# Kernel optimization log

Hardware: AMD Instinct MI355X
Metric: run time of the kernel (lower is better)

The kernel has to match this reference:

```python
import jax, jax.numpy as jnp
import numpy as np

B, S, D, H = 2, 2048, 1024, 16
HD = D // H

def setup_inputs() -> dict:
    key = jax.random.key(0)
    ks = jax.random.split(key, 6)
    s = 1.0 / np.sqrt(D)
    return {
        "inputs": jax.random.normal(ks[0], (B, S, D), dtype=jnp.float32),
        "Wq": jax.random.normal(ks[1], (D, D), dtype=jnp.float32) * s,
        "Wk": jax.random.normal(ks[2], (D, D), dtype=jnp.float32) * s,
        "Wv": jax.random.normal(ks[3], (D, D), dtype=jnp.float32) * s,
        "Wo": jax.random.normal(ks[4], (D, D), dtype=jnp.float32) * s,
        "bo": jax.random.normal(ks[5], (D,), dtype=jnp.float32) * 0.01,
    }

def reference(inputs, Wq, Wk, Wv, Wo, bo):
    b, n, _ = inputs.shape
    # Linear projections (torch Linear: x @ W.T), reshape to [b, H, n, hd]
    def proj(W):
        return (inputs @ W.T).reshape(b, n, H, HD).transpose(0, 2, 1, 3)
    q, k, v = proj(Wq), proj(Wk), proj(Wv)
    scores = jnp.einsum('bhqd,bhkd->bhqk', q, k)  # [b,H,n,n]
    causal = jnp.triu(jnp.ones((n, n), dtype=bool), k=1)
    scores = jnp.where(causal, -jnp.inf, scores)
    w = jax.nn.softmax(scores / np.sqrt(HD), axis=-1)
    ctx = jnp.einsum('bhqk,bhkd->bhqd', w, v)
    ctx = ctx.transpose(0, 2, 1, 3).reshape(b, n, D)
    return ctx @ Wo.T + bo
```

## Files before the change

### kernel.cpp

```cpp
#include <hip/hip_runtime.h>
#include <hip/hip_bf16.h>
#include <stdint.h>

#define B_   2
#define S_   2048
#define D_   1024
#define H_   16
#define LOG2E 1.4426950408889634f

using f32x4  = __attribute__((ext_vector_type(4))) float;
using short8 = __attribute__((ext_vector_type(8))) short;

__device__ __forceinline__ unsigned short f2bf(float x) {
    unsigned u = __builtin_bit_cast(unsigned, x);
    u += 0x7fffu + ((u >> 16) & 1u);
    return (unsigned short)(u >> 16);
}

__device__ __forceinline__ unsigned cvt_pk_bf16(float lo, float hi) {
    unsigned r;
    asm("v_cvt_pk_bf16_f32 %0, %1, %2" : "=v"(r) : "v"(lo), "v"(hi));
    return r;
}

__device__ __forceinline__ float fast_exp2(float x) {
    float r;
    asm("v_exp_f32 %0, %1" : "=v"(r) : "v"(x));
    return r;
}

__device__ __forceinline__ float fast_rcp(float x) {
    float r;
    asm("v_rcp_f32 %0, %1" : "=v"(r) : "v"(x));
    return r;
}

__device__ __forceinline__ void gll16(const void* g, void* l) {
    __builtin_amdgcn_global_load_lds(
        (const __attribute__((address_space(1))) void*)(uintptr_t)g,
        (__attribute__((address_space(3))) void*)(uint32_t)(uintptr_t)l,
        16, 0, 0);
}

#define MFMA_BF16(a, b, c) __builtin_amdgcn_mfma_f32_16x16x32_bf16((a), (b), (c), 0, 0, 0)

__global__ __launch_bounds__(256)
void conv_all_kernel(const float* __restrict__ X,
                     const float* __restrict__ Wq, const float* __restrict__ Wk,
                     const float* __restrict__ Wv, const float* __restrict__ Wo,
                     short* __restrict__ Xb, short* __restrict__ Wqkv,
                     short* __restrict__ Wob) {
    const int bid = blockIdx.x;
    const float* src;
    short* dst;
    float sc = 1.0f;
    int i;
    if (bid < 2048) {
        src = X; dst = Xb; i = bid * 256 + threadIdx.x;
    } else {
        int wv = bid - 2048;
        int which = wv >> 9;
        src = (which == 0) ? Wq : (which == 1) ? Wk : (which == 2) ? Wv : Wo;
        dst = (which == 3) ? Wob : (Wqkv + (size_t)which * D_ * D_);
        if (which == 0) sc = 0.125f * LOG2E;
        i = (wv & 511) * 256 + threadIdx.x;
    }
    const float4* s4 = (const float4*)src;
    float4 a = s4[i * 2];
    float4 b = s4[i * 2 + 1];
    union { unsigned short u[8]; short8 v; } o;
    o.u[0] = f2bf(a.x * sc); o.u[1] = f2bf(a.y * sc); o.u[2] = f2bf(a.z * sc); o.u[3] = f2bf(a.w * sc);
    o.u[4] = f2bf(b.x * sc); o.u[5] = f2bf(b.y * sc); o.u[6] = f2bf(b.z * sc); o.u[7] = f2bf(b.w * sc);
    ((short8*)dst)[i] = o.v;
}

__global__ __launch_bounds__(256, 3)
void gemm_qkv_m97_kernel(const short* __restrict__ X, const short* __restrict__ Wqkv,
                         short* __restrict__ Qo, short* __restrict__ Ko,
                         short* __restrict__ VTo)
{
    __shared__ short sA[128 * 64];
    __shared__ short sB[128 * 64];
    const int cid = blockIdx.x;
    const int swz = (cid & 7) * 96 + (cid >> 3);
    const int n0 = (swz % 24) * 128;
    const int m0 = (swz / 24) * 128;
    const int tid = threadIdx.x, lane = tid & 63, w = tid >> 6;
    const int wm = w & 1, wn = w >> 1;
    const int l15 = lane & 15, lg = lane >> 4;

    const f32x4 z4 = {0.f, 0.f, 0.f, 0.f};
    f32x4 acc[4][4];
    #pragma unroll
    for (int i = 0; i < 4; ++i)
        #pragma unroll
        for (int j = 0; j < 4; ++j) acc[i][j] = z4;

    for (int kt = 0; kt < 16; ++kt) {
        const int k0 = kt << 6;
        #pragma unroll
        for (int it = 0; it < 4; ++it) {
            int g = it * 256 + tid;
            int r = g >> 3, s = g & 7;
            int sb = s ^ (r & 7);
            int dst = (it * 256 + w * 64) * 16;
            gll16(X    + (size_t)(m0 + r) * D_ + k0 + sb * 8, (char*)sA + dst);
            gll16(Wqkv + (size_t)(n0 + r) * D_ + k0 + sb * 8, (char*)sB + dst);
        }
        __syncthreads();
        #pragma unroll
        for (int ks = 0; ks < 2; ++ks) {
            short8 af[4], bf[4];
            #pragma unroll
            for (int i = 0; i < 4; ++i) {
                int r = wm * 64 + i * 16 + l15;
                af[i] = *(const short8*)(sA + r * 64 + ((((ks << 2) + lg) ^ (r & 7)) << 3));
            }
            #pragma unroll
            for (int j = 0; j < 4; ++j) {
                int r = wn * 64 + j * 16 + l15;
                bf[j] = *(const short8*)(sB + r * 64 + ((((ks << 2) + lg) ^ (r & 7)) << 3));
            }
            __builtin_amdgcn_s_setprio(1);
            #pragma unroll
            for (int i = 0; i < 4; ++i)
                #pragma unroll
                for (int j = 0; j < 4; ++j)
                    acc[i][j] = MFMA_BF16(af[i], bf[j], acc[i][j]);
            __builtin_amdgcn_s_setprio(0);
        }
        __syncthreads();
    }

    const int z = n0 >> 10;
    if (z < 2) {
        short* Out = (z == 0) ? Qo : Ko;
        #pragma unroll
        for (int j = 0; j < 4; ++j) {
            int n = n0 + wn * 64 + j * 16 + l15;
            int h = (n >> 6) & 15, hd = n & 63;
            #pragma unroll
            for (int i = 0; i < 4; ++i)
                #pragma unroll
                for (int r = 0; r < 4; ++r) {
                    int m = m0 + wm * 64 + i * 16 + lg * 4 + r;
                    int b = m >> 11, s = m & (S_ - 1);
                    Out[(((size_t)b * H_ + h) * S_ + s) * 64 + hd] = (short)f2bf(acc[i][j][r]);
                }
        }
    } else {
        #pragma unroll
        for (int j = 0; j < 4; ++j) {
            int n = n0 + wn * 64 + j * 16 + l15;
            int h = (n >> 6) & 15, hd = n & 63;
            #pragma unroll
            for (int i = 0; i < 4; ++i) {
                int m = m0 + wm * 64 + i * 16 + lg * 4;
                int b = m >> 11, s0 = m & (S_ - 1);
                union { unsigned u32[2]; unsigned long long q64; } pk;
                pk.u32[0] = cvt_pk_bf16(acc[i][j][0], acc[i][j][1]);
                pk.u32[1] = cvt_pk_bf16(acc[i][j][2], acc[i][j][3]);
                *(unsigned long long*)(VTo + (((size_t)b * H_ + h) * 64 + hd) * S_ + s0) = pk.q64;
            }
        }
    }
}

__global__ __launch_bounds__(512, 4)
void gemm_out_kernel(const short* __restrict__ CTX, const short* __restrict__ Wob,
                     const float* __restrict__ bias, float* __restrict__ out)
{
    __shared__ short sA[2][128 * 64];
    __shared__ short sB[2][128 * 64];
    const int cid = blockIdx.y * 8 + blockIdx.x;
    const int swz = (cid & 7) * 32 + (cid >> 3);
    const int n0 = (swz & 7) * 128;
    const int m0 = (swz >> 3) * 128;
    const int tid = threadIdx.x, lane = tid & 63, w = tid >> 6;
    const int wm = w >> 2, wn = w & 3;
    const int l15 = lane & 15, lg = lane >> 4;

#define STAGE_O(buf, kt) do {                                                  \
        int k0_ = (kt) << 6;                                                   \
        _Pragma("unroll")                                                      \
        for (int it_ = 0; it_ < 2; ++it_) {                                    \
            int g_ = it_ * 512 + tid;                                          \
            int r_ = g_ >> 3, s_ = g_ & 7;                                     \
            int sb_ = s_ ^ (r_ & 7);                                           \
            int dst_ = (it_ * 512 + w * 64) * 16;                              \
            gll16(CTX + (size_t)(m0 + r_) * D_ + k0_ + sb_ * 8,                \
                  (char*)sA[buf] + dst_);                                      \
            gll16(Wob + (size_t)(n0 + r_) * D_ + k0_ + sb_ * 8,                \
                  (char*)sB[buf] + dst_);                                      \
        }                                                                      \
    } while (0)

    const f32x4 z4 = {0.f, 0.f, 0.f, 0.f};
    f32x4 acc[4][2];
    #pragma unroll
    for (int i = 0; i < 4; ++i)
        #pragma unroll
        for (int j = 0; j < 2; ++j) acc[i][j] = z4;

    STAGE_O(0, 0);
    STAGE_O(1, 1);

    for (int t = 0; t < 16; ++t) {
        if (t < 15) { asm volatile("s_waitcnt vmcnt(4)" ::: "memory"); }
        else        { asm volatile("s_waitcnt vmcnt(0)" ::: "memory"); }
        __builtin_amdgcn_sched_barrier(0);
        __builtin_amdgcn_s_barrier();
        __builtin_amdgcn_sched_barrier(0);
        const short* a  = sA[t & 1];
        const short* bm = sB[t & 1];
        #pragma unroll
        for (int ks = 0; ks < 2; ++ks) {
            short8 af[4], bf[2];
            #pragma unroll
            for (int i = 0; i < 4; ++i) {
                int r = wm * 64 + i * 16 + l15;
                af[i] = *(const short8*)(a + r * 64 + ((((ks << 2) + lg) ^ (r & 7)) << 3));
            }
            #pragma unroll
            for (int j = 0; j < 2; ++j) {
                int r = wn * 32 + j * 16 + l15;
                bf[j] = *(const short8*)(bm + r * 64 + ((((ks << 2) + lg) ^ (r & 7)) << 3));
            }
            __builtin_amdgcn_s_setprio(1);
            #pragma unroll
            for (int i = 0; i < 4; ++i)
                #pragma unroll
                for (int j = 0; j < 2; ++j)
                    acc[i][j] = MFMA_BF16(af[i], bf[j], acc[i][j]);
            __builtin_amdgcn_s_setprio(0);
        }
        asm volatile("s_waitcnt lgkmcnt(0)" ::: "memory");
        __builtin_amdgcn_sched_barrier(0);
        __builtin_amdgcn_s_barrier();
        __builtin_amdgcn_sched_barrier(0);
        if (t + 2 < 16) STAGE_O(t & 1, t + 2);
    }
#undef STAGE_O

    #pragma unroll
    for (int j = 0; j < 2; ++j) {
        int n = n0 + wn * 32 + j * 16 + l15;
        float bn = bias[n];
        #pragma unroll
        for (int i = 0; i < 4; ++i)
            #pragma unroll
            for (int r = 0; r < 4; ++r) {
                int m = m0 + wm * 64 + i * 16 + lg * 4 + r;
                out[(size_t)m * D_ + n] = acc[i][j][r] + bn;
            }
    }
}

__global__ __launch_bounds__(256, 4)
void attn_kernel(const short* __restrict__ Q, const short* __restrict__ K,
                 const short* __restrict__ VT, short* __restrict__ CTX)
{
    __shared__ short Kb[2][4096];
    __shared__ short Vb[2][4096];
    __shared__ char  Pl[4 * 2048];
    const int idx = blockIdx.x;
    const int k4  = idx >> 8;
    const int u   = idx & 255;
    const int v   = u >> 5;
    const int bh  = u & 31;
    const int ht  = (k4 == 0) ? v : (k4 == 1) ? (15 - v)
                  : (k4 == 2) ? (16 + v) : (31 - v);
    const int b  = bh >> 4, h = bh & 15;
    const int tid = threadIdx.x, lane = tid & 63, w = tid >> 6;
    const int l15 = lane & 15, lg = lane >> 4;
    const short* Qg = Q  + (size_t)bh * S_ * 64;
    const short* Kg = K  + (size_t)bh * S_ * 64;
    const short* Vg = VT + (size_t)bh * 64 * S_;
    char* Pw = Pl + w * 2048;

    const int qb = ht * 64 + w * 16;
    const int nt = ht + 1;

#define STAGE_KV(bufidx, ktile) do {                                         \
        int kt64_ = (ktile) << 6;                                            \
        _Pragma("unroll")                                                    \
        for (int it_ = 0; it_ < 2; ++it_) {                                  \
            int g_ = it_ * 256 + tid;                                        \
            int row_ = g_ >> 3, jb_ = g_ & 7;                                \
            int sj_ = jb_ ^ (row_ & 7);                                      \
            int base_ = (it_ * 256 + w * 64) * 16;                           \
            gll16(Kg + (size_t)(kt64_ + row_) * 64 + sj_ * 8,                \
                  (char*)Kb[bufidx] + base_);                                \
            gll16(Vg + (size_t)row_ * S_ + kt64_ + sj_ * 8,                  \
                  (char*)Vb[bufidx] + base_);                                \
        }                                                                    \
    } while (0)

    short8 qf[2];
    #pragma unroll
    for (int ks = 0; ks < 2; ++ks)
        qf[ks] = *(const short8*)(Qg + (size_t)(qb + l15) * 64 + ks * 32 + lg * 8);

    const short8 ones8 = { (short)0x3F80, (short)0x3F80, (short)0x3F80, (short)0x3F80,
                           (short)0x3F80, (short)0x3F80, (short)0x3F80, (short)0x3F80 };
    const f32x4 z4 = {0.f, 0.f, 0.f, 0.f};
    f32x4 o[4];
    f32x4 o5 = z4;
    #pragma unroll
    for (int nf = 0; nf < 4; ++nf) o[nf] = z4;

    STAGE_KV(0, 0);
    STAGE_KV(1, 1);

    for (int t = 0; t < nt; ++t) {
        if (t + 1 < nt) { asm volatile("s_waitcnt vmcnt(4)" ::: "memory"); }
        else            { asm volatile("s_waitcnt vmcnt(0)" ::: "memory"); }
        __builtin_amdgcn_sched_barrier(0);
        __builtin_amdgcn_s_barrier();
        __builtin_amdgcn_sched_barrier(0);
        const short* kb = Kb[t & 1];
        const short* vb = Vb[t & 1];
        const int kt = t << 6;

        {
            f32x4 sv[4] = {z4, z4, z4, z4};
            __builtin_amdgcn_s_setprio(1);
            #pragma unroll
            for (int ks = 0; ks < 2; ++ks)
                #pragma unroll
                for (int nf = 0; nf < 4; ++nf) {
                    int rr = nf * 16 + l15;
                    short8 kf = *(const short8*)((const char*)kb + rr * 128 +
                                                 (((ks << 2) + lg) ^ (rr & 7)) * 16);
                    sv[nf] = MFMA_BF16(kf, qf[ks], sv[nf]);
                }
            __builtin_amdgcn_s_setprio(0);
            if (kt + 63 > qb) {
                int q = qb + l15;
                #pragma unroll
                for (int nf = 0; nf < 4; ++nf)
                    #pragma unroll
                    for (int r = 0; r < 4; ++r)
                        if (kt + nf * 16 + lg * 4 + r > q) sv[nf][r] = -3e38f;
            }
            #pragma unroll
            for (int nf = 0; nf < 4; ++nf)
                #pragma unroll
                for (int r = 0; r < 4; ++r)
                    sv[nf][r] = fast_exp2(sv[nf][r]);
            #pragma unroll
            for (int nf = 0; nf < 4; ++nf) {
                union { unsigned u32[2]; unsigned long long q64; } pk;
                pk.u32[0] = cvt_pk_bf16(sv[nf][0], sv[nf][1]);
                pk.u32[1] = cvt_pk_bf16(sv[nf][2], sv[nf][3]);
                int kby = (nf * 16 + lg * 4) * 2;
                int off = l15 * 128 + (((kby >> 4) ^ (l15 & 7)) << 4) + (kby & 15);
                *(unsigned long long*)(Pw + off) = pk.q64;
            }
            #pragma unroll
            for (int ks = 0; ks < 2; ++ks) {
                int off = l15 * 128 + ((((ks << 2) + lg) ^ (l15 & 7)) << 4);
                short8 af = *(const short8*)(Pw + off);
                __builtin_amdgcn_s_setprio(1);
                #pragma unroll
                for (int nf = 0; nf < 4; ++nf) {
                    int rr = nf * 16 + l15;
                    short8 vf = *(const short8*)((const char*)vb + rr * 128 +
                                                 (((ks << 2) + lg) ^ (rr & 7)) * 16);
                    o[nf] = MFMA_BF16(af, vf, o[nf]);
                }
                o5 = MFMA_BF16(af, ones8, o5);
                __builtin_amdgcn_s_setprio(0);
            }
        }
        asm volatile("s_waitcnt lgkmcnt(0)" ::: "memory");
        __builtin_amdgcn_sched_barrier(0);
        __builtin_amdgcn_s_barrier();
        __builtin_amdgcn_sched_barrier(0);
        if (t + 2 < nt) STAGE_KV(t & 1, t + 2);
    }
#undef STAGE_KV

    #pragma unroll
    for (int r = 0; r < 4; ++r) {
        float inv = fast_rcp(o5[r]);
        int s = qb + lg * 4 + r;
        size_t base = ((size_t)b * S_ + s) * D_ + h * 64;
        #pragma unroll
        for (int nf = 0; nf < 4; ++nf)
            CTX[base + nf * 16 + l15] = (short)f2bf(o[nf][r] * inv);
    }
}

extern "C" void kernel_launch(void* const* d_in, const int* in_sizes, int n_in,
                              void* d_out, int out_size, void* d_ws, size_t ws_size,
                              hipStream_t stream) {
    const float* X  = (const float*)d_in[0];
    const float* Wq = (const float*)d_in[1];
    const float* Wk = (const float*)d_in[2];
    const float* Wv = (const float*)d_in[3];
    const float* Wo = (const float*)d_in[4];
    const float* bo = (const float*)d_in[5];
    float* out = (float*)d_out;

    char* ws = (char*)d_ws;
    const size_t MB = 1024 * 1024;
    short* Xb   = (short*)(ws);
    short* CTXw = (short*)(ws);
    short* Wqkv = (short*)(ws +  8 * MB);
    short* Wob  = (short*)(ws + 14 * MB);
    short* Qw   = (short*)(ws + 16 * MB);
    short* Kw   = (short*)(ws + 24 * MB);
    short* VTw  = (short*)(ws + 32 * MB);

    conv_all_kernel<<<4096, 256, 0, stream>>>(X, Wq, Wk, Wv, Wo, Xb, Wqkv, Wob);

    gemm_qkv_m97_kernel<<<768, 256, 0, stream>>>(Xb, Wqkv, Qw, Kw, VTw);

    attn_kernel<<<1024, 256, 0, stream>>>(Qw, Kw, VTw, CTXw);

    gemm_out_kernel<<<dim3(8, 32), 512, 0, stream>>>(CTXw, Wob, bo, out);
}
```

Measured before the change: 86.42 us.

## Double-buffer QKV GEMM with K=32 stages and async prefetch

The QKV projection GEMM now stages K in 32-wide slices into two LDS buffers and prefetches two slices ahead, waiting on vmcnt so global loads overlap MFMA work. Before, it loaded a 64-wide K tile and then stalled at a barrier on every iteration. The LDS footprint stays the same, but there are twice as many iterations, each with two barriers and a new XOR swizzle for the 32-wide rows. That swizzle could introduce bank conflicts.

New measurement: 91.60 us. +6.0%, slower.

```diff
diff --git a/kernel.cpp b/kernel.cpp
--- a/kernel.cpp
+++ b/kernel.cpp
@@ -75,12 +75,12 @@
 }
 
 __global__ __launch_bounds__(256, 3)
-void gemm_qkv_m97_kernel(const short* __restrict__ X, const short* __restrict__ Wqkv,
-                         short* __restrict__ Qo, short* __restrict__ Ko,
-                         short* __restrict__ VTo)
+void gemm_qkv32_kernel(const short* __restrict__ X, const short* __restrict__ Wqkv,
+                       short* __restrict__ Qo, short* __restrict__ Ko,
+                       short* __restrict__ VTo)
 {
-    __shared__ short sA[128 * 64];
-    __shared__ short sB[128 * 64];
+    __shared__ short sA[2][128 * 32];
+    __shared__ short sB[2][128 * 32];
     const int cid = blockIdx.x;
     const int swz = (cid & 7) * 96 + (cid >> 3);
     const int n0 = (swz % 24) * 128;
@@ -89,6 +89,21 @@
     const int wm = w & 1, wn = w >> 1;
     const int l15 = lane & 15, lg = lane >> 4;
 
+#define STAGE_K(buf, kt) do {                                                  \
+        int k0_ = (kt) << 5;                                                   \
+        _Pragma("unroll")                                                      \
+        for (int it_ = 0; it_ < 2; ++it_) {                                    \
+            int g_ = it_ * 256 + tid;                                          \
+            int r_ = g_ >> 2, s_ = g_ & 3;                                     \
+            int sb_ = s_ ^ ((r_ >> 1) & 3);                                    \
+            int dst_ = (it_ * 256 + w * 64) * 16;                              \
+            gll16(X    + (size_t)(m0 + r_) * D_ + k0_ + sb_ * 8,               \
+                  (char*)sA[buf] + dst_);                                      \
+            gll16(Wqkv + (size_t)(n0 + r_) * D_ + k0_ + sb_ * 8,               \
+                  (char*)sB[buf] + dst_);                                      \
+        }                                                                      \
+    } while (0)
+
     const f32x4 z4 = {0.f, 0.f, 0.f, 0.f};
     f32x4 acc[4][4];
     #pragma unroll
@@ -96,41 +111,42 @@
         #pragma unroll
         for (int j = 0; j < 4; ++j) acc[i][j] = z4;
 
-    for (int kt = 0; kt < 16; ++kt) {
-        const int k0 = kt << 6;
-        #pragma unroll
-        for (int it = 0; it < 4; ++it) {
-            int g = it * 256 + tid;
-            int r = g >> 3, s = g & 7;
-            int sb = s ^ (r & 7);
-            int dst = (it * 256 + w * 64) * 16;
-            gll16(X    + (size_t)(m0 + r) * D_ + k0 + sb * 8, (char*)sA + dst);
-            gll16(Wqkv + (size_t)(n0 + r) * D_ + k0 + sb * 8, (char*)sB + dst);
-        }
-        __syncthreads();
-        #pragma unroll
-        for (int ks = 0; ks < 2; ++ks) {
-            short8 af[4], bf[4];
-            #pragma unroll
-            for (int i = 0; i < 4; ++i) {
-                int r = wm * 64 + i * 16 + l15;
-                af[i] = *(const short8*)(sA + r * 64 + ((((ks << 2) + lg) ^ (r & 7)) << 3));
-            }
-            #pragma unroll
-            for (int j = 0; j < 4; ++j) {
-                int r = wn * 64 + j * 16 + l15;
-                bf[j] = *(const short8*)(sB + r * 64 + ((((ks << 2) + lg) ^ (r & 7)) << 3));
-            }
-            __builtin_amdgcn_s_setprio(1);
-            #pragma unroll
-            for (int i = 0; i < 4; ++i)
-                #pragma unroll
-                for (int j = 0; j < 4; ++j)
-                    acc[i][j] = MFMA_BF16(af[i], bf[j], acc[i][j]);
-            __builtin_amdgcn_s_setprio(0);
-        }
-        __syncthreads();
-    }
+    STAGE_K(0, 0);
+    STAGE_K(1, 1);
+
+    for (int t = 0; t < 32; ++t) {
+        if (t < 31) { asm volatile("s_waitcnt vmcnt(4)" ::: "memory"); }
+        else        { asm volatile("s_waitcnt vmcnt(0)" ::: "memory"); }
+        __builtin_amdgcn_sched_barrier(0);
+        __builtin_amdgcn_s_barrier();
+        __builtin_amdgcn_sched_barrier(0);
+        const short* a  = sA[t & 1];
+        const short* bm = sB[t & 1];
+        short8 af[4], bf[4];
+        #pragma unroll
+        for (int i = 0; i < 4; ++i) {
+            int r = wm * 64 + i * 16 + l15;
+            af[i] = *(const short8*)(a + r * 32 + ((lg ^ ((r >> 1) & 3)) << 3));
+        }
+        #pragma unroll
+        for (int j = 0; j < 4; ++j) {
+            int r = wn * 64 + j * 16 + l15;
+            bf[j] = *(const short8*)(bm + r * 32 + ((lg ^ ((r >> 1) & 3)) << 3));
+        }
+        __builtin_amdgcn_s_setprio(1);
+        #pragma unroll
+        for (int i = 0; i < 4; ++i)
+            #pragma unroll
+            for (int j = 0; j < 4; ++j)
+                acc[i][j] = MFMA_BF16(af[i], bf[j], acc[i][j]);
+        __builtin_amdgcn_s_setprio(0);
+        asm volatile("s_waitcnt lgkmcnt(0)" ::: "memory");
+        __builtin_amdgcn_sched_barrier(0);
+        __builtin_amdgcn_s_barrier();
+        __builtin_amdgcn_sched_barrier(0);
+        if (t + 2 < 32) STAGE_K(t & 1, t + 2);
+    }
+#undef STAGE_K
 
     const int z = n0 >> 10;
     if (z < 2) {
@@ -415,7 +431,7 @@
 
     conv_all_kernel<<<4096, 256, 0, stream>>>(X, Wq, Wk, Wv, Wo, Xb, Wqkv, Wob);
 
-    gemm_qkv_m97_kernel<<<768, 256, 0, stream>>>(Xb, Wqkv, Qw, Kw, VTw);
+    gemm_qkv32_kernel<<<768, 256, 0, stream>>>(Xb, Wqkv, Qw, Kw, VTw);
 
     attn_kernel<<<1024, 256, 0, stream>>>(Qw, Kw, VTw, CTXw);
 
```

## Process 128 query rows per attention block to reuse staged K/V tiles

Applied to the files above, without the earlier changes.

Each wave of the attention kernel now handles 32 query rows instead of 16, so a block covers 128 rows and the grid is halved to 512 blocks. Every K/V tile staged in shared memory feeds twice as many MFMAs, which halves K/V global traffic and staging per query. Waves skip key tiles that lie entirely above their causal diagonal. The cost is more registers (launch bounds lowered to 2 blocks per SM), doubled P scratch in shared memory, fewer blocks, and coarser causal load balance.

After: 88.68 us. 2.6% more time.

```diff
diff --git a/kernel.cpp b/kernel.cpp
--- a/kernel.cpp
+++ b/kernel.cpp
@@ -256,30 +256,29 @@
     }
 }
 
-__global__ __launch_bounds__(256, 4)
+__global__ __launch_bounds__(256, 2)
 void attn_kernel(const short* __restrict__ Q, const short* __restrict__ K,
                  const short* __restrict__ VT, short* __restrict__ CTX)
 {
     __shared__ short Kb[2][4096];
     __shared__ short Vb[2][4096];
-    __shared__ char  Pl[4 * 2048];
+    __shared__ char  Pl[4 * 4096];
     const int idx = blockIdx.x;
-    const int k4  = idx >> 8;
+    const int k2  = idx >> 8;
     const int u   = idx & 255;
     const int v   = u >> 5;
     const int bh  = u & 31;
-    const int ht  = (k4 == 0) ? v : (k4 == 1) ? (15 - v)
-                  : (k4 == 2) ? (16 + v) : (31 - v);
+    const int ft  = k2 ? (15 - v) : v;
     const int b  = bh >> 4, h = bh & 15;
     const int tid = threadIdx.x, lane = tid & 63, w = tid >> 6;
     const int l15 = lane & 15, lg = lane >> 4;
     const short* Qg = Q  + (size_t)bh * S_ * 64;
     const short* Kg = K  + (size_t)bh * S_ * 64;
     const short* Vg = VT + (size_t)bh * 64 * S_;
-    char* Pw = Pl + w * 2048;
-
-    const int qb = ht * 64 + w * 16;
-    const int nt = ht + 1;
+    char* Pw = Pl + w * 4096;
+
+    const int qb = ft * 128 + w * 32;
+    const int nt = 2 * ft + 2;
 
 #define STAGE_KV(bufidx, ktile) do {                                         \
         int kt64_ = (ktile) << 6;                                            \
@@ -296,18 +295,20 @@
         }                                                                    \
     } while (0)
 
-    short8 qf[2];
-    #pragma unroll
-    for (int ks = 0; ks < 2; ++ks)
-        qf[ks] = *(const short8*)(Qg + (size_t)(qb + l15) * 64 + ks * 32 + lg * 8);
+    short8 qf[2][2];
+    #pragma unroll
+    for (int mf = 0; mf < 2; ++mf)
+        #pragma unroll
+        for (int ks = 0; ks < 2; ++ks)
+            qf[mf][ks] = *(const short8*)(Qg + (size_t)(qb + mf * 16 + l15) * 64 + ks * 32 + lg * 8);
 
     const short8 ones8 = { (short)0x3F80, (short)0x3F80, (short)0x3F80, (short)0x3F80,
                            (short)0x3F80, (short)0x3F80, (short)0x3F80, (short)0x3F80 };
     const f32x4 z4 = {0.f, 0.f, 0.f, 0.f};
-    f32x4 o[4];
-    f32x4 o5 = z4;
-    #pragma unroll
-    for (int nf = 0; nf < 4; ++nf) o[nf] = z4;
+    f32x4 o0[4], o1[4];
+    f32x4 o5a = z4, o5b = z4;
+    #pragma unroll
+    for (int nf = 0; nf < 4; ++nf) { o0[nf] = z4; o1[nf] = z4; }
 
     STAGE_KV(0, 0);
     STAGE_KV(1, 1);
@@ -322,8 +323,9 @@
         const short* vb = Vb[t & 1];
         const int kt = t << 6;
 
-        {
-            f32x4 sv[4] = {z4, z4, z4, z4};
+        if (kt <= qb + 31) {
+            f32x4 sv0[4] = {z4, z4, z4, z4};
+            f32x4 sv1[4] = {z4, z4, z4, z4};
             __builtin_amdgcn_s_setprio(1);
             #pragma unroll
             for (int ks = 0; ks < 2; ++ks)
@@ -332,7 +334,8 @@
                     int rr = nf * 16 + l15;
                     short8 kf = *(const short8*)((const char*)kb + rr * 128 +
                                                  (((ks << 2) + lg) ^ (rr & 7)) * 16);
-                    sv[nf] = MFMA_BF16(kf, qf[ks], sv[nf]);
+                    sv0[nf] = MFMA_BF16(kf, qf[0][ks], sv0[nf]);
+                    sv1[nf] = MFMA_BF16(kf, qf[1][ks], sv1[nf]);
                 }
             __builtin_amdgcn_s_setprio(0);
             if (kt + 63 > qb) {
@@ -341,35 +344,51 @@
                 for (int nf = 0; nf < 4; ++nf)
                     #pragma unroll
                     for (int r = 0; r < 4; ++r)
-                        if (kt + nf * 16 + lg * 4 + r > q) sv[nf][r] = -3e38f;
+                        if (kt + nf * 16 + lg * 4 + r > q) sv0[nf][r] = -3e38f;
+            }
+            if (kt + 63 > qb + 16) {
+                int q = qb + 16 + l15;
+                #pragma unroll
+                for (int nf = 0; nf < 4; ++nf)
+                    #pragma unroll
+                    for (int r = 0; r < 4; ++r)
+                        if (kt + nf * 16 + lg * 4 + r > q) sv1[nf][r] = -3e38f;
             }
             #pragma unroll
             for (int nf = 0; nf < 4; ++nf)
                 #pragma unroll
-                for (int r = 0; r < 4; ++r)
-                    sv[nf][r] = fast_exp2(sv[nf][r]);
+                for (int r = 0; r < 4; ++r) {
+                    sv0[nf][r] = fast_exp2(sv0[nf][r]);
+                    sv1[nf][r] = fast_exp2(sv1[nf][r]);
+                }
             #pragma unroll
             for (int nf = 0; nf < 4; ++nf) {
-                union { unsigned u32[2]; unsigned long long q64; } pk;
-                pk.u32[0] = cvt_pk_bf16(sv[nf][0], sv[nf][1]);
-                pk.u32[1] = cvt_pk_bf16(sv[nf][2], sv[nf][3]);
                 int kby = (nf * 16 + lg * 4) * 2;
                 int off = l15 * 128 + (((kby >> 4) ^ (l15 & 7)) << 4) + (kby & 15);
+                union { unsigned u32[2]; unsigned long long q64; } pk;
+                pk.u32[0] = cvt_pk_bf16(sv0[nf][0], sv0[nf][1]);
+                pk.u32[1] = cvt_pk_bf16(sv0[nf][2], sv0[nf][3]);
                 *(unsigned long long*)(Pw + off) = pk.q64;
+                pk.u32[0] = cvt_pk_bf16(sv1[nf][0], sv1[nf][1]);
+                pk.u32[1] = cvt_pk_bf16(sv1[nf][2], sv1[nf][3]);
+                *(unsigned long long*)(Pw + 2048 + off) = pk.q64;
             }
             #pragma unroll
             for (int ks = 0; ks < 2; ++ks) {
                 int off = l15 * 128 + ((((ks << 2) + lg) ^ (l15 & 7)) << 4);
-                short8 af = *(const short8*)(Pw + off);
+                short8 af0 = *(const short8*)(Pw + off);
+                short8 af1 = *(const short8*)(Pw + 2048 + off);
                 __builtin_amdgcn_s_setprio(1);
                 #pragma unroll
                 for (int nf = 0; nf < 4; ++nf) {
                     int rr = nf * 16 + l15;
                     short8 vf = *(const short8*)((const char*)vb + rr * 128 +
                                                  (((ks << 2) + lg) ^ (rr & 7)) * 16);
-                    o[nf] = MFMA_BF16(af, vf, o[nf]);
+                    o0[nf] = MFMA_BF16(af0, vf, o0[nf]);
+                    o1[nf] = MFMA_BF16(af1, vf, o1[nf]);
                 }
-                o5 = MFMA_BF16(af, ones8, o5);
+                o5a = MFMA_BF16(af0, ones8, o5a);
+                o5b = MFMA_BF16(af1, ones8, o5b);
                 __builtin_amdgcn_s_setprio(0);
             }
         }
@@ -383,12 +402,21 @@
 
     #pragma unroll
     for (int r = 0; r < 4; ++r) {
-        float inv = fast_rcp(o5[r]);
+        float inv = fast_rcp(o5a[r]);
         int s = qb + lg * 4 + r;
         size_t base = ((size_t)b * S_ + s) * D_ + h * 64;
         #pragma unroll
         for (int nf = 0; nf < 4; ++nf)
-            CTX[base + nf * 16 + l15] = (short)f2bf(o[nf][r] * inv);
+            CTX[base + nf * 16 + l15] = (short)f2bf(o0[nf][r] * inv);
+    }
+    #pragma unroll
+    for (int r = 0; r < 4; ++r) {
+        float inv = fast_rcp(o5b[r]);
+        int s = qb + 16 + lg * 4 + r;
+        size_t base = ((size_t)b * S_ + s) * D_ + h * 64;
+        #pragma unroll
+        for (int nf = 0; nf < 4; ++nf)
+            CTX[base + nf * 16 + l15] = (short)f2bf(o1[nf][r] * inv);
     }
 }
 
@@ -417,7 +445,7 @@
 
     gemm_qkv_m97_kernel<<<768, 256, 0, stream>>>(Xb, Wqkv, Qw, Kw, VTw);
 
-    attn_kernel<<<1024, 256, 0, stream>>>(Qw, Kw, VTw, CTXw);
+    attn_kernel<<<512, 256, 0, stream>>>(Qw, Kw, VTw, CTXw);
 
     gemm_out_kernel<<<dim3(8, 32), 512, 0, stream>>>(CTXw, Wob, bo, out);
 }
```
